# Performance work log

Measured on AMD Instinct MI355X. Metric: run time of the kernel, lower is better.

## Reference

```python
import jax, jax.numpy as jnp
import numpy as np
import math

EMBED_DIM = 1024
NUM_HEADS = 16
HEAD_DIM = EMBED_DIM // NUM_HEADS
B, T = 2, 2048


def setup_inputs() -> dict:
    key = jax.random.key(0)
    ks = jax.random.split(key, 8)
    x = jax.random.normal(ks[0], (B, T, EMBED_DIM), dtype=jnp.float32)
    context_vector = jax.random.normal(ks[1], (B, T, EMBED_DIM), dtype=jnp.float32)
    # causal mask: 1 where attention allowed, 0 elsewhere (mask==0 -> -1e9)
    mask = jnp.tril(jnp.ones((T, T), dtype=jnp.int32))[None, None, :, :]
    # Xavier-uniform projections (fan_in = fan_out = EMBED_DIM)
    limit = math.sqrt(6.0 / (EMBED_DIM + EMBED_DIM))
    def xavier(k):
        return jax.random.uniform(k, (EMBED_DIM, EMBED_DIM), jnp.float32, -limit, limit)
    w_q = xavier(ks[2])
    w_k = xavier(ks[3])
    w_v = xavier(ks[4])
    w_o = xavier(ks[5])
    b_o = jnp.zeros((EMBED_DIM,), jnp.float32)
    context_bias = jnp.zeros((EMBED_DIM,), jnp.float32)
    return {"x": x, "mask": mask, "context_vector": context_vector,
            "w_q": w_q, "w_k": w_k, "w_v": w_v, "w_o": w_o, "b_o": b_o,
            "context_bias": context_bias}


def reference(x, mask, context_vector, w_q, w_k, w_v, w_o, b_o, context_bias):
    Bx, Tx, C = x.shape
    H, hd = NUM_HEADS, HEAD_DIM
    # nn.Linear: y = x @ W^T
    q = x @ w_q.T + context_bias * context_vector  # [B,T,C]
    k = x @ w_k.T
    v = x @ w_v.T
    q = q.reshape(Bx, Tx, H, hd).transpose(0, 2, 1, 3)  # [B,H,T,hd]
    k = k.reshape(Bx, Tx, H, hd).transpose(0, 2, 1, 3)
    v = v.reshape(Bx, Tx, H, hd).transpose(0, 2, 1, 3)
    scores = jnp.einsum('bhqd,bhkd->bhqk', q, k) / math.sqrt(hd)  # [B,H,T,T]
    scores = jnp.where(mask == 0, jnp.float32(-1e9), scores)
    attn = jax.nn.softmax(scores, axis=-1)  # dropout p=0 (eval) -> identity
    out = jnp.einsum('bhqk,bhkd->bhqd', attn, v)  # [B,H,T,hd]
    out = out.transpose(0, 2, 1, 3).reshape(Bx, Tx, C)
    return out @ w_o.T + b_o
```

## Files before the change

kernel.cpp:

```cpp
#include <hip/hip_runtime.h>

typedef __bf16 bf16_t;
typedef __attribute__((ext_vector_type(8))) __bf16 bf16x8;
typedef __attribute__((ext_vector_type(4))) __bf16 bf16x4;
typedef __attribute__((ext_vector_type(2))) __bf16 bf16x2;
typedef __attribute__((ext_vector_type(4))) float floatx4;
typedef __attribute__((ext_vector_type(4))) unsigned uintx4;

#define LOG2E 1.4426950408889634f

__device__ __forceinline__ void async16(const void* g, void* l) {
  __builtin_amdgcn_global_load_lds(
      (const __attribute__((address_space(1))) void*)g,
      (__attribute__((address_space(3))) void*)l, 16, 0, 0);
}

__global__ __launch_bounds__(256) void cast_all(
    const float* __restrict__ x, const float* __restrict__ wq,
    const float* __restrict__ wk, const float* __restrict__ wv,
    const float* __restrict__ wo, bf16_t* __restrict__ dst) {
  int i = (blockIdx.x * 256 + threadIdx.x) * 4;
  const float* src;
  int off;
  if (i < 4194304) {
    src = x; off = i;
  } else {
    int j = i - 4194304;
    int w = j >> 20;
    off = j & 1048575;
    src = (w == 0) ? wq : (w == 1) ? wk : (w == 2) ? wv : wo;
  }
  float4 v = *(const float4*)(src + off);
  bf16x4 o;
  o[0] = (bf16_t)v.x; o[1] = (bf16_t)v.y; o[2] = (bf16_t)v.z; o[3] = (bf16_t)v.w;
  *(bf16x4*)(dst + i) = o;
}

__device__ __forceinline__ void gemm64x128(const bf16_t* __restrict__ A,
                                           const bf16_t* __restrict__ W,
                                           int tileM, int tileN, char* smem,
                                           floatx4 acc[2][4]) {
  bf16_t* As = (bf16_t*)smem;
  bf16_t* Bs = (bf16_t*)(smem + 8192);
  const int tid = threadIdx.x;
  const int lane = tid & 63;
  const int quad = lane >> 4;
  const int l15 = lane & 15;
  const int wid = tid >> 6;
  const int waveM = (wid >> 1) * 32;
  const int waveN = (wid & 1) * 64;
  const int swz = l15 & 7;
  for (int i = 0; i < 2; ++i)
    for (int j = 0; j < 4; ++j)
      for (int r = 0; r < 4; ++r) acc[i][j][r] = 0.0f;

  const int r0 = tid >> 3;
  const int sc = ((tid & 7) ^ (r0 & 7)) << 3;
  const size_t abase = (size_t)(tileM + r0) * 1024 + sc;
  const size_t bbase = (size_t)(tileN + r0) * 1024 + sc;
  const int ldbase = (tid & ~63) * 16;

  for (int kt = 0; kt < 1024; kt += 64) {
    if (kt) __syncthreads();
    for (int j = 0; j < 2; ++j)
      async16(A + abase + (size_t)j * 32 * 1024 + kt, smem + j * 4096 + ldbase);
    for (int j = 0; j < 4; ++j)
      async16(W + bbase + (size_t)j * 32 * 1024 + kt, smem + 8192 + j * 4096 + ldbase);
    __syncthreads();
    for (int kk = 0; kk < 2; ++kk) {
      const int cq = (((kk << 2) + quad) ^ swz) << 3;
      bf16x8 af[2], bfr[4];
      for (int rb = 0; rb < 2; ++rb)
        af[rb] = *(const bf16x8*)&As[(waveM + rb * 16 + l15) * 64 + cq];
      for (int cb = 0; cb < 4; ++cb)
        bfr[cb] = *(const bf16x8*)&Bs[(waveN + cb * 16 + l15) * 64 + cq];
      for (int rb = 0; rb < 2; ++rb)
        for (int cb = 0; cb < 4; ++cb)
          acc[rb][cb] = __builtin_amdgcn_mfma_f32_16x16x32_bf16(af[rb], bfr[cb],
                                                                acc[rb][cb], 0, 0, 0);
    }
  }
}

__global__ __launch_bounds__(256) void proj_qkv(
    const bf16_t* __restrict__ xb, const bf16_t* __restrict__ wq,
    const bf16_t* __restrict__ wk, const bf16_t* __restrict__ wv,
    const float* __restrict__ cbias, const float* __restrict__ cv,
    bf16_t* __restrict__ qb, bf16_t* __restrict__ kb, bf16_t* __restrict__ vtb) {
  __shared__ __align__(16) char smem[24576];
  const int mode = blockIdx.z;
  const bf16_t* W = (mode == 0) ? wq : ((mode == 1) ? wk : wv);
  const int tileM = blockIdx.y * 64, tileN = blockIdx.x * 128;
  floatx4 acc[2][4];
  gemm64x128(xb, W, tileM, tileN, smem, acc);
  const int tid = threadIdx.x, lane = tid & 63, quad = lane >> 4, l15 = lane & 15,
            wid = tid >> 6;
  const int waveM = (wid >> 1) * 32, waveN = (wid & 1) * 64;
  bf16_t* T = (bf16_t*)smem;
  __syncthreads();
  for (int rb = 0; rb < 2; ++rb)
    for (int cb = 0; cb < 4; ++cb)
      for (int r = 0; r < 4; ++r) {
        int rl = waveM + rb * 16 + quad * 4 + r;
        int cl = waveN + cb * 16 + l15;
        float v = acc[rb][cb][r];
        if (mode == 0)
          v += cbias[tileN + cl] * cv[(size_t)(tileM + rl) * 1024 + tileN + cl];
        if (mode == 2)
          T[cl * 72 + (waveM + quad * 8 + rb * 4 + r)] = (bf16_t)v;
        else
          T[rl * 136 + cl] = (bf16_t)v;
      }
  __syncthreads();
  if (mode == 2) {
    const int rowi = tid >> 1, half = tid & 1;
    const bf16_t* src = T + rowi * 72 + half * 32;
    int n = tileN + rowi;
    int b = tileM >> 11;
    int t0 = (tileM & 2047) + half * 32;
    bf16_t* dst = vtb + ((size_t)b * 1024 + n) * 2048 + t0;
    for (int i = 0; i < 4; ++i) *(bf16x8*)(dst + i * 8) = *(const bf16x8*)(src + i * 8);
  } else {
    const int rowi = tid >> 2, qtr = tid & 3;
    const bf16_t* src = T + rowi * 136 + qtr * 32;
    int tg = tileM + rowi;
    int b = tg >> 11, t = tg & 2047;
    int n0 = tileN + qtr * 32;
    int h = n0 >> 6;
    bf16_t* base = (mode == 0) ? qb : kb;
    bf16_t* dst = base + ((size_t)(b * 16 + h) * 2048 + t) * 64 + (n0 & 63);
    for (int i = 0; i < 4; ++i) *(bf16x8*)(dst + i * 8) = *(const bf16x8*)(src + i * 8);
  }
}

__global__ __launch_bounds__(256) void attn_fwd(
    const bf16_t* __restrict__ qb, const bf16_t* __restrict__ kb,
    const bf16_t* __restrict__ vtb, bf16_t* __restrict__ ob) {
  __shared__ __align__(16) bf16_t Qs[64 * 64];
  __shared__ __align__(16) bf16_t Ks[2][64 * 64];
  __shared__ __align__(16) bf16_t Vs[2][64 * 64];
  const int bh = blockIdx.x;
  const int qt = 31 - blockIdx.y;
  const int q0 = qt * 64;
  const int tid = threadIdx.x, lane = tid & 63, w = tid >> 6, quad = lane >> 4,
            l15 = lane & 15;

  const int sr = tid >> 3;
  const int sc = (tid & 7) ^ (sr & 7);
  const int ldst = (tid & ~63) * 16;
  const int swz = l15 & 7;

  {
    const bf16_t* gq = qb + ((size_t)bh * 2048 + q0 + sr) * 64 + sc * 8;
    async16(gq, (char*)Qs + ldst);
    async16(gq + 32 * 64, (char*)Qs + ldst + 4096);
  }

  floatx4 O[4];
  for (int d = 0; d < 4; ++d)
    for (int r = 0; r < 4; ++r) O[d][r] = 0.f;
  float m_c = -1e30f, l_c = 0.f;
  const float SC = 0.125f * LOG2E;
  const floatx4 zero4 = {0.f, 0.f, 0.f, 0.f};

  {
    const bf16_t* gk = kb + ((size_t)bh * 2048 + sr) * 64 + sc * 8;
    async16(gk, (char*)Ks[0] + ldst);
    async16(gk + 32 * 64, (char*)Ks[0] + ldst + 4096);
    const bf16_t* gv = vtb + ((size_t)bh * 64 + sr) * 2048 + sc * 8;
    async16(gv, (char*)Vs[0] + ldst);
    async16(gv + (size_t)32 * 2048, (char*)Vs[0] + ldst + 4096);
  }
  __syncthreads();

  bf16x8 qf[2];
  for (int ks = 0; ks < 2; ++ks) {
    const int cq = (ks * 4 + quad) ^ swz;
    qf[ks] = *(const bf16x8*)&Qs[(w * 16 + l15) * 64 + cq * 8];
  }

  for (int kt = 0; kt <= qt; ++kt) {
    const int cur = kt & 1;
    if (kt < qt) {
      const int nxt = cur ^ 1;
      const bf16_t* gk2 = kb + ((size_t)bh * 2048 + (kt + 1) * 64 + sr) * 64 + sc * 8;
      async16(gk2, (char*)Ks[nxt] + ldst);
      async16(gk2 + 32 * 64, (char*)Ks[nxt] + ldst + 4096);
      const bf16_t* gv2 = vtb + ((size_t)bh * 64 + sr) * 2048 + (size_t)(kt + 1) * 64 + sc * 8;
      async16(gv2, (char*)Vs[nxt] + ldst);
      async16(gv2 + (size_t)32 * 2048, (char*)Vs[nxt] + ldst + 4096);
    }
    floatx4 s[4];
    {
      const int cq0 = (quad ^ swz) << 3;
      const int cq1 = ((4 + quad) ^ swz) << 3;
      for (int kbt = 0; kbt < 4; ++kbt) {
        bf16x8 kf0 = *(const bf16x8*)&Ks[cur][(kbt * 16 + l15) * 64 + cq0];
        s[kbt] = __builtin_amdgcn_mfma_f32_16x16x32_bf16(kf0, qf[0], zero4, 0, 0, 0);
      }
      for (int kbt = 0; kbt < 4; ++kbt) {
        bf16x8 kf1 = *(const bf16x8*)&Ks[cur][(kbt * 16 + l15) * 64 + cq1];
        s[kbt] = __builtin_amdgcn_mfma_f32_16x16x32_bf16(kf1, qf[1], s[kbt], 0, 0, 0);
      }
    }
    if (kt == qt) {
      const int qloc = w * 16 + l15;
      for (int kbt = 0; kbt < 4; ++kbt)
        for (int r = 0; r < 4; ++r)
          if (kbt * 16 + quad * 4 + r > qloc) s[kbt][r] = -1e30f;
    }
    float mx = s[0][0];
    for (int i = 0; i < 4; ++i)
      for (int r = 0; r < 4; ++r) mx = fmaxf(mx, s[i][r]);
    mx = fmaxf(mx, __shfl_xor(mx, 16));
    mx = fmaxf(mx, __shfl_xor(mx, 32));
    const float m_new = fmaxf(m_c, mx);
    const float alpha = exp2f((m_c - m_new) * SC);
    const float msc = m_new * SC;
    m_c = m_new;
    float p[4][4];
    float rs = 0.f;
    for (int i = 0; i < 4; ++i)
      for (int r = 0; r < 4; ++r) {
        float v = exp2f(fmaf(s[i][r], SC, -msc));
        p[i][r] = v;
        rs += v;
      }
    rs += __shfl_xor(rs, 16);
    rs += __shfl_xor(rs, 32);
    l_c = l_c * alpha + rs;
    for (int db = 0; db < 4; ++db)
      for (int r = 0; r < 4; ++r) O[db][r] *= alpha;
    unsigned pk[4][2];
    for (int i = 0; i < 4; ++i)
      for (int rr = 0; rr < 2; ++rr) {
        bf16x2 t2;
        t2[0] = (bf16_t)p[i][2 * rr];
        t2[1] = (bf16_t)p[i][2 * rr + 1];
        pk[i][rr] = __builtin_bit_cast(unsigned, t2);
      }
    for (int c = 0; c < 2; ++c) {
      uintx4 bw;
      bw[0] = pk[2 * c][0];
      bw[1] = pk[2 * c][1];
      bw[2] = pk[2 * c + 1][0];
      bw[3] = pk[2 * c + 1][1];
      bf16x8 pfrag = __builtin_bit_cast(bf16x8, bw);
      const int cqv = (((c << 2) + quad) ^ swz) << 3;
      for (int db = 0; db < 4; ++db) {
        bf16x8 vf = *(const bf16x8*)&Vs[cur][(db * 16 + l15) * 64 + cqv];
        O[db] = __builtin_amdgcn_mfma_f32_16x16x32_bf16(vf, pfrag, O[db], 0, 0, 0);
      }
    }
    __syncthreads();
  }
  const int b = bh >> 4, h = bh & 15;
  const float inv = 1.0f / l_c;
  const int t = q0 + w * 16 + l15;
  for (int db = 0; db < 4; ++db) {
    bf16x4 o4;
    for (int r = 0; r < 4; ++r) o4[r] = (bf16_t)(O[db][r] * inv);
    *(bf16x4*)&ob[((size_t)b * 2048 + t) * 1024 + h * 64 + db * 16 + quad * 4] = o4;
  }
}

__global__ __launch_bounds__(256) void proj_o(
    const bf16_t* __restrict__ ain, const bf16_t* __restrict__ wo,
    const float* __restrict__ bo, float* __restrict__ out) {
  __shared__ __align__(16) char smem[24576];
  const int tileM = blockIdx.y * 64, tileN = blockIdx.x * 128;
  floatx4 acc[2][4];
  gemm64x128(ain, wo, tileM, tileN, smem, acc);
  const int tid = threadIdx.x, lane = tid & 63, quad = lane >> 4, l15 = lane & 15,
            wid = tid >> 6;
  const int waveM = (wid >> 1) * 32, waveN = (wid & 1) * 64;
  for (int rb = 0; rb < 2; ++rb)
    for (int cb = 0; cb < 4; ++cb)
      for (int r = 0; r < 4; ++r) {
        int row = tileM + waveM + rb * 16 + quad * 4 + r;
        int col = tileN + waveN + cb * 16 + l15;
        out[(size_t)row * 1024 + col] = acc[rb][cb][r] + bo[col];
      }
}

extern "C" void kernel_launch(void* const* d_in, const int* in_sizes, int n_in,
                              void* d_out, int out_size, void* d_ws, size_t ws_size,
                              hipStream_t stream) {
  const float* x     = (const float*)d_in[0];
  const float* cv    = (const float*)d_in[2];
  const float* wq    = (const float*)d_in[3];
  const float* wk    = (const float*)d_in[4];
  const float* wv    = (const float*)d_in[5];
  const float* wo    = (const float*)d_in[6];
  const float* bo    = (const float*)d_in[7];
  const float* cbias = (const float*)d_in[8];
  float* out = (float*)d_out;

  char* ws = (char*)d_ws;
  const size_t MB = 1 << 20;
  bf16_t* xb  = (bf16_t*)(ws + 0 * MB);
  bf16_t* wqb = (bf16_t*)(ws + 8 * MB);
  bf16_t* wkb = (bf16_t*)(ws + 10 * MB);
  bf16_t* wvb = (bf16_t*)(ws + 12 * MB);
  bf16_t* wob = (bf16_t*)(ws + 14 * MB);
  bf16_t* qb  = (bf16_t*)(ws + 16 * MB);
  bf16_t* kb  = (bf16_t*)(ws + 24 * MB);
  bf16_t* vtb = (bf16_t*)(ws + 32 * MB);
  bf16_t* ob  = (bf16_t*)(ws + 40 * MB);

  cast_all<<<8192, 256, 0, stream>>>(x, wq, wk, wv, wo, xb);
  proj_qkv<<<dim3(8, 64, 3), 256, 0, stream>>>(xb, wqb, wkb, wvb, cbias, cv, qb, kb, vtb);
  attn_fwd<<<dim3(32, 32), 256, 0, stream>>>(qb, kb, vtb, ob);
  proj_o<<<dim3(8, 64), 256, 0, stream>>>(ob, wob, bo, out);
}
```

Measured before the change: 214.4 us.

## Pair causal query tiles per block to balance work and share K/V loads

```diff
diff --git a/kernel.cpp b/kernel.cpp
--- a/kernel.cpp
+++ b/kernel.cpp
@@ -136,12 +136,12 @@
 __global__ __launch_bounds__(256) void attn_fwd(
     const bf16_t* __restrict__ qb, const bf16_t* __restrict__ kb,
     const bf16_t* __restrict__ vtb, bf16_t* __restrict__ ob) {
-  __shared__ __align__(16) bf16_t Qs[64 * 64];
   __shared__ __align__(16) bf16_t Ks[2][64 * 64];
   __shared__ __align__(16) bf16_t Vs[2][64 * 64];
   const int bh = blockIdx.x;
-  const int qt = 31 - blockIdx.y;
-  const int q0 = qt * 64;
+  const int p = blockIdx.y;
+  const int qta = p, qtb = 31 - p;
+  const int q0a = qta * 64, q0b = qtb * 64;
   const int tid = threadIdx.x, lane = tid & 63, w = tid >> 6, quad = lane >> 4,
             l15 = lane & 15;
 
@@ -151,19 +151,12 @@
   const int swz = l15 & 7;
 
   {
-    const bf16_t* gq = qb + ((size_t)bh * 2048 + q0 + sr) * 64 + sc * 8;
-    async16(gq, (char*)Qs + ldst);
-    async16(gq + 32 * 64, (char*)Qs + ldst + 4096);
-  }
-
-  floatx4 O[4];
-  for (int d = 0; d < 4; ++d)
-    for (int r = 0; r < 4; ++r) O[d][r] = 0.f;
-  float m_c = -1e30f, l_c = 0.f;
-  const float SC = 0.125f * LOG2E;
-  const floatx4 zero4 = {0.f, 0.f, 0.f, 0.f};
-
-  {
+    const bf16_t* gqa = qb + ((size_t)bh * 2048 + q0a + sr) * 64 + sc * 8;
+    async16(gqa, (char*)Ks[1] + ldst);
+    async16(gqa + 32 * 64, (char*)Ks[1] + ldst + 4096);
+    const bf16_t* gqb = qb + ((size_t)bh * 2048 + q0b + sr) * 64 + sc * 8;
+    async16(gqb, (char*)Vs[1] + ldst);
+    async16(gqb + 32 * 64, (char*)Vs[1] + ldst + 4096);
     const bf16_t* gk = kb + ((size_t)bh * 2048 + sr) * 64 + sc * 8;
     async16(gk, (char*)Ks[0] + ldst);
     async16(gk + 32 * 64, (char*)Ks[0] + ldst + 4096);
@@ -173,15 +166,25 @@
   }
   __syncthreads();
 
-  bf16x8 qf[2];
+  bf16x8 qfa[2], qfb[2];
   for (int ks = 0; ks < 2; ++ks) {
-    const int cq = (ks * 4 + quad) ^ swz;
-    qf[ks] = *(const bf16x8*)&Qs[(w * 16 + l15) * 64 + cq * 8];
-  }
-
-  for (int kt = 0; kt <= qt; ++kt) {
+    const int cq = ((ks * 4 + quad) ^ swz) << 3;
+    qfa[ks] = *(const bf16x8*)&Ks[1][(w * 16 + l15) * 64 + cq];
+    qfb[ks] = *(const bf16x8*)&Vs[1][(w * 16 + l15) * 64 + cq];
+  }
+  __syncthreads();
+
+  floatx4 Oa[4], Ob[4];
+  for (int d = 0; d < 4; ++d)
+    for (int r = 0; r < 4; ++r) { Oa[d][r] = 0.f; Ob[d][r] = 0.f; }
+  float m_a = -1e30f, l_a = 0.f, m_b = -1e30f, l_b = 0.f;
+  const float SC = 0.125f * LOG2E;
+  const floatx4 zero4 = {0.f, 0.f, 0.f, 0.f};
+  const int qloc = w * 16 + l15;
+
+  for (int kt = 0; kt <= qtb; ++kt) {
     const int cur = kt & 1;
-    if (kt < qt) {
+    if (kt < qtb) {
       const int nxt = cur ^ 1;
       const bf16_t* gk2 = kb + ((size_t)bh * 2048 + (kt + 1) * 64 + sr) * 64 + sc * 8;
       async16(gk2, (char*)Ks[nxt] + ldst);
@@ -190,77 +193,134 @@
       async16(gv2, (char*)Vs[nxt] + ldst);
       async16(gv2 + (size_t)32 * 2048, (char*)Vs[nxt] + ldst + 4096);
     }
-    floatx4 s[4];
+    const bool doA = (kt <= qta);
+    floatx4 sa[4], sb[4];
     {
       const int cq0 = (quad ^ swz) << 3;
       const int cq1 = ((4 + quad) ^ swz) << 3;
       for (int kbt = 0; kbt < 4; ++kbt) {
         bf16x8 kf0 = *(const bf16x8*)&Ks[cur][(kbt * 16 + l15) * 64 + cq0];
-        s[kbt] = __builtin_amdgcn_mfma_f32_16x16x32_bf16(kf0, qf[0], zero4, 0, 0, 0);
+        sb[kbt] = __builtin_amdgcn_mfma_f32_16x16x32_bf16(kf0, qfb[0], zero4, 0, 0, 0);
+        if (doA)
+          sa[kbt] = __builtin_amdgcn_mfma_f32_16x16x32_bf16(kf0, qfa[0], zero4, 0, 0, 0);
       }
       for (int kbt = 0; kbt < 4; ++kbt) {
         bf16x8 kf1 = *(const bf16x8*)&Ks[cur][(kbt * 16 + l15) * 64 + cq1];
-        s[kbt] = __builtin_amdgcn_mfma_f32_16x16x32_bf16(kf1, qf[1], s[kbt], 0, 0, 0);
-      }
-    }
-    if (kt == qt) {
-      const int qloc = w * 16 + l15;
-      for (int kbt = 0; kbt < 4; ++kbt)
+        sb[kbt] = __builtin_amdgcn_mfma_f32_16x16x32_bf16(kf1, qfb[1], sb[kbt], 0, 0, 0);
+        if (doA)
+          sa[kbt] = __builtin_amdgcn_mfma_f32_16x16x32_bf16(kf1, qfa[1], sa[kbt], 0, 0, 0);
+      }
+    }
+    if (kt == qtb)
+      for (int i = 0; i < 4; ++i)
         for (int r = 0; r < 4; ++r)
-          if (kbt * 16 + quad * 4 + r > qloc) s[kbt][r] = -1e30f;
-    }
-    float mx = s[0][0];
-    for (int i = 0; i < 4; ++i)
-      for (int r = 0; r < 4; ++r) mx = fmaxf(mx, s[i][r]);
-    mx = fmaxf(mx, __shfl_xor(mx, 16));
-    mx = fmaxf(mx, __shfl_xor(mx, 32));
-    const float m_new = fmaxf(m_c, mx);
-    const float alpha = exp2f((m_c - m_new) * SC);
-    const float msc = m_new * SC;
-    m_c = m_new;
-    float p[4][4];
-    float rs = 0.f;
-    for (int i = 0; i < 4; ++i)
-      for (int r = 0; r < 4; ++r) {
-        float v = exp2f(fmaf(s[i][r], SC, -msc));
-        p[i][r] = v;
-        rs += v;
-      }
-    rs += __shfl_xor(rs, 16);
-    rs += __shfl_xor(rs, 32);
-    l_c = l_c * alpha + rs;
+          if (i * 16 + quad * 4 + r > qloc) sb[i][r] = -1e30f;
+    if (kt == qta)
+      for (int i = 0; i < 4; ++i)
+        for (int r = 0; r < 4; ++r)
+          if (i * 16 + quad * 4 + r > qloc) sa[i][r] = -1e30f;
+
+    unsigned pkb[4][2];
+    float alphab;
+    {
+      float mx = sb[0][0];
+      for (int i = 0; i < 4; ++i)
+        for (int r = 0; r < 4; ++r) mx = fmaxf(mx, sb[i][r]);
+      mx = fmaxf(mx, __shfl_xor(mx, 16));
+      mx = fmaxf(mx, __shfl_xor(mx, 32));
+      const float m_new = fmaxf(m_b, mx);
+      alphab = exp2f((m_b - m_new) * SC);
+      const float msc = m_new * SC;
+      m_b = m_new;
+      float rs = 0.f;
+      for (int i = 0; i < 4; ++i) {
+        float p0 = exp2f(fmaf(sb[i][0], SC, -msc));
+        float p1 = exp2f(fmaf(sb[i][1], SC, -msc));
+        float p2 = exp2f(fmaf(sb[i][2], SC, -msc));
+        float p3 = exp2f(fmaf(sb[i][3], SC, -msc));
+        rs += (p0 + p1) + (p2 + p3);
+        bf16x2 t0; t0[0] = (bf16_t)p0; t0[1] = (bf16_t)p1;
+        bf16x2 t1; t1[0] = (bf16_t)p2; t1[1] = (bf16_t)p3;
+        pkb[i][0] = __builtin_bit_cast(unsigned, t0);
+        pkb[i][1] = __builtin_bit_cast(unsigned, t1);
+      }
+      rs += __shfl_xor(rs, 16);
+      rs += __shfl_xor(rs, 32);
+      l_b = l_b * alphab + rs;
+    }
+    unsigned pka[4][2];
+    float alphaa = 1.f;
+    if (doA) {
+      float mx = sa[0][0];
+      for (int i = 0; i < 4; ++i)
+        for (int r = 0; r < 4; ++r) mx = fmaxf(mx, sa[i][r]);
+      mx = fmaxf(mx, __shfl_xor(mx, 16));
+      mx = fmaxf(mx, __shfl_xor(mx, 32));
+      const float m_new = fmaxf(m_a, mx);
+      alphaa = exp2f((m_a - m_new) * SC);
+      const float msc = m_new * SC;
+      m_a = m_new;
+      float rs = 0.f;
+      for (int i = 0; i < 4; ++i) {
+        float p0 = exp2f(fmaf(sa[i][0], SC, -msc));
+        float p1 = exp2f(fmaf(sa[i][1], SC, -msc));
+        float p2 = exp2f(fmaf(sa[i][2], SC, -msc));
+        float p3 = exp2f(fmaf(sa[i][3], SC, -msc));
+        rs += (p0 + p1) + (p2 + p3);
+        bf16x2 t0; t0[0] = (bf16_t)p0; t0[1] = (bf16_t)p1;
+        bf16x2 t1; t1[0] = (bf16_t)p2; t1[1] = (bf16_t)p3;
+        pka[i][0] = __builtin_bit_cast(unsigned, t0);
+        pka[i][1] = __builtin_bit_cast(unsigned, t1);
+      }
+      rs += __shfl_xor(rs, 16);
+      rs += __shfl_xor(rs, 32);
+      l_a = l_a * alphaa + rs;
+      for (int db = 0; db < 4; ++db)
+        for (int r = 0; r < 4; ++r) Oa[db][r] *= alphaa;
+    }
     for (int db = 0; db < 4; ++db)
-      for (int r = 0; r < 4; ++r) O[db][r] *= alpha;
-    unsigned pk[4][2];
-    for (int i = 0; i < 4; ++i)
-      for (int rr = 0; rr < 2; ++rr) {
-        bf16x2 t2;
-        t2[0] = (bf16_t)p[i][2 * rr];
-        t2[1] = (bf16_t)p[i][2 * rr + 1];
-        pk[i][rr] = __builtin_bit_cast(unsigned, t2);
-      }
+      for (int r = 0; r < 4; ++r) Ob[db][r] *= alphab;
+
     for (int c = 0; c < 2; ++c) {
-      uintx4 bw;
-      bw[0] = pk[2 * c][0];
-      bw[1] = pk[2 * c][1];
-      bw[2] = pk[2 * c + 1][0];
-      bw[3] = pk[2 * c + 1][1];
-      bf16x8 pfrag = __builtin_bit_cast(bf16x8, bw);
+      uintx4 bwb;
+      bwb[0] = pkb[2 * c][0]; bwb[1] = pkb[2 * c][1];
+      bwb[2] = pkb[2 * c + 1][0]; bwb[3] = pkb[2 * c + 1][1];
+      bf16x8 pfb = __builtin_bit_cast(bf16x8, bwb);
+      bf16x8 pfa;
+      if (doA) {
+        uintx4 bwa;
+        bwa[0] = pka[2 * c][0]; bwa[1] = pka[2 * c][1];
+        bwa[2] = pka[2 * c + 1][0]; bwa[3] = pka[2 * c + 1][1];
+        pfa = __builtin_bit_cast(bf16x8, bwa);
+      }
       const int cqv = (((c << 2) + quad) ^ swz) << 3;
       for (int db = 0; db < 4; ++db) {
         bf16x8 vf = *(const bf16x8*)&Vs[cur][(db * 16 + l15) * 64 + cqv];
-        O[db] = __builtin_amdgcn_mfma_f32_16x16x32_bf16(vf, pfrag, O[db], 0, 0, 0);
+        Ob[db] = __builtin_amdgcn_mfma_f32_16x16x32_bf16(vf, pfb, Ob[db], 0, 0, 0);
+        if (doA)
+          Oa[db] = __builtin_amdgcn_mfma_f32_16x16x32_bf16(vf, pfa, Oa[db], 0, 0, 0);
       }
     }
     __syncthreads();
   }
   const int b = bh >> 4, h = bh & 15;
-  const float inv = 1.0f / l_c;
-  const int t = q0 + w * 16 + l15;
-  for (int db = 0; db < 4; ++db) {
-    bf16x4 o4;
-    for (int r = 0; r < 4; ++r) o4[r] = (bf16_t)(O[db][r] * inv);
-    *(bf16x4*)&ob[((size_t)b * 2048 + t) * 1024 + h * 64 + db * 16 + quad * 4] = o4;
+  {
+    const float inv = 1.0f / l_a;
+    const int t = q0a + w * 16 + l15;
+    for (int db = 0; db < 4; ++db) {
+      bf16x4 o4;
+      for (int r = 0; r < 4; ++r) o4[r] = (bf16_t)(Oa[db][r] * inv);
+      *(bf16x4*)&ob[((size_t)b * 2048 + t) * 1024 + h * 64 + db * 16 + quad * 4] = o4;
+    }
+  }
+  {
+    const float inv = 1.0f / l_b;
+    const int t = q0b + w * 16 + l15;
+    for (int db = 0; db < 4; ++db) {
+      bf16x4 o4;
+      for (int r = 0; r < 4; ++r) o4[r] = (bf16_t)(Ob[db][r] * inv);
+      *(bf16x4*)&ob[((size_t)b * 2048 + t) * 1024 + h * 64 + db * 16 + quad * 4] = o4;
+    }
   }
 }
 
@@ -310,6 +370,6 @@
 
   cast_all<<<8192, 256, 0, stream>>>(x, wq, wk, wv, wo, xb);
   proj_qkv<<<dim3(8, 64, 3), 256, 0, stream>>>(xb, wqb, wkb, wvb, cbias, cv, qb, kb, vtb);
-  attn_fwd<<<dim3(32, 32), 256, 0, stream>>>(qb, kb, vtb, ob);
+  attn_fwd<<<dim3(32, 16), 256, 0, stream>>>(qb, kb, vtb, ob);
   proj_o<<<dim3(8, 64), 256, 0, stream>>>(ob, wob, bo, out);
 }
```

Result: slower. 230.4 us (+7.5%).
